# Kernel optimization log

Hardware: AMD Instinct MI355X
Metric: run time of the kernel (lower is better)

Reference implementation:

```python
import jax, jax.numpy as jnp
import numpy as np
import math

N_EMBD = 1024
N_HEAD = 16
HEAD_DIM = N_EMBD // N_HEAD // 2  # 32
DEPTH = 1
LAMBDA_INIT = 0.8 - 0.6 * math.exp(-0.3 * (DEPTH - 1))  # 0.2
EPS = 1e-5


def setup_inputs() -> dict:
    key = jax.random.key(0)
    ks = jax.random.split(key, 8)
    B, T, C = 4, 1024, N_EMBD
    x = jax.random.normal(ks[0], (B, T, C), dtype=jnp.float32)
    w_attn = jax.random.normal(ks[1], (C, 3 * C), dtype=jnp.float32) * (1.0 / math.sqrt(C))
    w_proj = jax.random.normal(ks[2], (C, C), dtype=jnp.float32) * (1.0 / math.sqrt(C))
    lambda_q1 = jax.random.normal(ks[3], (HEAD_DIM,), dtype=jnp.float32) * 0.1
    lambda_q2 = jax.random.normal(ks[4], (HEAD_DIM,), dtype=jnp.float32) * 0.1
    lambda_k1 = jax.random.normal(ks[5], (HEAD_DIM,), dtype=jnp.float32) * 0.1
    lambda_k2 = jax.random.normal(ks[6], (HEAD_DIM,), dtype=jnp.float32) * 0.1
    gamma = jnp.ones((2 * HEAD_DIM,), dtype=jnp.float32)  # RMSNorm affine weight
    return {"x": x, "w_attn": w_attn, "w_proj": w_proj,
            "lambda_q1": lambda_q1, "lambda_q2": lambda_q2,
            "lambda_k1": lambda_k1, "lambda_k2": lambda_k2, "gamma": gamma}


def reference(x, w_attn, w_proj, lambda_q1, lambda_q2, lambda_k1, lambda_k2, gamma):
    B, T, C = x.shape
    H, hd = N_HEAD, HEAD_DIM
    qkv = x @ w_attn                                  # [B,T,3C]
    q, k, v = jnp.split(qkv, 3, axis=-1)
    q = q.reshape(B, T, 2 * H, hd).transpose(0, 2, 1, 3)   # [B,2H,T,hd]
    k = k.reshape(B, T, 2 * H, hd).transpose(0, 2, 1, 3)   # [B,2H,T,hd]
    v = v.reshape(B, T, H, 2 * hd).transpose(0, 2, 1, 3)   # [B,H,T,2hd]
    q = q * (hd ** -0.5)
    att = jnp.einsum('bhtd,bhsd->bhts', q, k) * (1.0 / math.sqrt(hd))
    causal = jnp.tril(jnp.ones((T, T), dtype=bool))
    att = jnp.where(causal, att, -jnp.inf)
    att = jax.nn.softmax(att, axis=-1)                # [B,2H,T,T]
    lam1 = jnp.exp(jnp.sum(lambda_q1 * lambda_k1))
    lam2 = jnp.exp(jnp.sum(lambda_q2 * lambda_k2))
    lambda_full = lam1 - lam2 + LAMBDA_INIT
    att = att.reshape(B, H, 2, T, T)
    att = att[:, :, 0] - lambda_full * att[:, :, 1]   # [B,H,T,T]
    out = jnp.einsum('bhts,bhsd->bhtd', att, v)       # [B,H,T,2hd]
    # RMSNorm over last dim with affine weight
    rms = jax.lax.rsqrt(jnp.mean(out * out, axis=-1, keepdims=True) + EPS)
    out = out * rms * gamma
    out = (1.0 - LAMBDA_INIT) * out
    out = out.transpose(0, 2, 1, 3).reshape(B, T, C)
    return out @ w_proj
```

## Files before the change

kernel.cpp:

```cpp
#include <hip/hip_runtime.h>

typedef unsigned short u16;
typedef unsigned int u32;
typedef __bf16 bf16x8 __attribute__((ext_vector_type(8)));
typedef float f32x4 __attribute__((ext_vector_type(4)));
typedef u16 u16x8 __attribute__((ext_vector_type(8)));
typedef u16 u16x4 __attribute__((ext_vector_type(4)));

#define DEV static __device__ __forceinline__

struct MaskT { static constexpr bool value = true; };
struct NoMaskT { static constexpr bool value = false; };

DEV u16 f2bf(float f) {
  unsigned u = __builtin_bit_cast(unsigned, f);
  u += 0x7fffu + ((u >> 16) & 1u);
  return (u16)(u >> 16);
}
DEV u16 f2bf_fast(float f) {
  unsigned u = __builtin_bit_cast(unsigned, f);
  return (u16)((u + 0x8000u) >> 16);
}
DEV float fexp2(float x) {
  float r;
  asm("v_exp_f32 %0, %1" : "=v"(r) : "v"(x));
  return r;
}

DEV void gld16(const void* g, void* l) {
  __builtin_amdgcn_global_load_lds((__attribute__((address_space(1))) void*)(g),
                                   (__attribute__((address_space(3))) void*)(l),
                                   16, 0, 0);
}

__global__ __launch_bounds__(256) void k_cast(const float* __restrict__ in,
                                              u16* __restrict__ out, int n4) {
  int i = blockIdx.x * 256 + threadIdx.x;
  if (i >= n4) return;
  float4 v = ((const float4*)in)[i];
  u16x4 r = { f2bf(v.x), f2bf(v.y), f2bf(v.z), f2bf(v.w) };
  ((u16x4*)out)[i] = r;
}

__global__ __launch_bounds__(256) void k_transpose_cast(const float* __restrict__ in,
                                                        u16* __restrict__ out,
                                                        int R, int Cc) {
  __shared__ u16 tile[64][65];
  int r0 = blockIdx.x * 64, c0 = blockIdx.y * 64;
  int tid = threadIdx.x;
#pragma unroll
  for (int rr = 0; rr < 4; ++rr) {
    int r = rr * 16 + (tid >> 4);
    int c = (tid & 15) * 4;
    float4 v = *(const float4*)&in[(size_t)(r0 + r) * Cc + c0 + c];
    tile[r][c + 0] = f2bf(v.x); tile[r][c + 1] = f2bf(v.y);
    tile[r][c + 2] = f2bf(v.z); tile[r][c + 3] = f2bf(v.w);
  }
  __syncthreads();
#pragma unroll
  for (int rr = 0; rr < 2; ++rr) {
    int cr = rr * 32 + (tid >> 3);
    int rc = (tid & 7) * 8;
    u16x8 v;
#pragma unroll
    for (int j = 0; j < 8; ++j) v[j] = tile[rc + j][cr];
    *(u16x8*)&out[(size_t)(c0 + cr) * R + r0 + rc] = v;
  }
}

__global__ __launch_bounds__(256) void k_vtrans(const u16* __restrict__ qkv,
                                                u16* __restrict__ vt) {
  __shared__ u16 tile[64][65];
  int bid = blockIdx.x;
  int b = bid >> 8, h = (bid >> 4) & 15, tt = bid & 15;
  int tid = threadIdx.x;
#pragma unroll
  for (int rr = 0; rr < 2; ++rr) {
    int tl = rr * 32 + (tid >> 3);
    int d0 = (tid & 7) * 8;
    u16x8 v = *(const u16x8*)&qkv[(size_t)(b * 1024 + tt * 64 + tl) * 3072 + 2048 + h * 64 + d0];
#pragma unroll
    for (int j = 0; j < 8; ++j) tile[tl][d0 + j] = v[j];
  }
  __syncthreads();
#pragma unroll
  for (int rr = 0; rr < 2; ++rr) {
    int d = rr * 32 + (tid >> 3);
    int t0 = (tid & 7) * 8;
    u16x8 v;
#pragma unroll
    for (int j = 0; j < 8; ++j) v[j] = tile[t0 + j][d];
    *(u16x8*)&vt[((size_t)(b * 16 + h) * 64 + d) * 1024 + tt * 64 + t0] = v;
  }
}

__global__ void k_lambda(const float* lq1, const float* lq2,
                         const float* lk1, const float* lk2, float* out) {
  int i = threadIdx.x;
  float a = 0.f, b = 0.f;
  if (i < 32) { a = lq1[i] * lk1[i]; b = lq2[i] * lk2[i]; }
#pragma unroll
  for (int s = 1; s < 64; s <<= 1) { a += __shfl_xor(a, s); b += __shfl_xor(b, s); }
  if (i == 0) out[0] = __expf(a) - __expf(b) + 0.2f;
}

template <bool OUT_F32>
__global__ __launch_bounds__(256) void k_gemm(const u16* __restrict__ A,
                                              const u16* __restrict__ Bt,
                                              void* __restrict__ Cout,
                                              int M, int N, int K) {
  __shared__ __align__(16) u16 As[2][128 * 32];
  __shared__ __align__(16) u16 Bs[2][128 * 32];
  int tid = threadIdx.x;
  int nbn = N >> 7;
  int wg = ((int)blockIdx.x & 7) * ((int)gridDim.x >> 3) + ((int)blockIdx.x >> 3);
  int bm = wg / nbn, bn = wg % nbn;
  int m0 = bm << 7, n0 = bn << 7;
  int lane = tid & 63, w = tid >> 6, wm = w >> 1, wn = w & 1;
  int lr = lane & 15, lg = lane >> 4;
  const u16* pA0; const u16* pA1; const u16* pB0; const u16* pB1;
  {
    int i0 = tid, i1 = tid + 256;
    int r0 = i0 >> 2, s80 = (i0 & 3) ^ ((r0 >> 1) & 3);
    int r1 = i1 >> 2, s81 = (i1 & 3) ^ ((r1 >> 1) & 3);
    pA0 = &A[(size_t)(m0 + r0) * K + s80 * 8];
    pA1 = &A[(size_t)(m0 + r1) * K + s81 * 8];
    pB0 = &Bt[(size_t)(n0 + r0) * K + s80 * 8];
    pB1 = &Bt[(size_t)(n0 + r1) * K + s81 * 8];
  }
  f32x4 acc[4][4] = {};
  auto stage = [&](int kt, int buf) {
    gld16(pA0 + kt, &As[buf][tid * 8]);
    gld16(pA1 + kt, &As[buf][(tid + 256) * 8]);
    gld16(pB0 + kt, &Bs[buf][tid * 8]);
    gld16(pB1 + kt, &Bs[buf][(tid + 256) * 8]);
  };
  int NK = K >> 5;
  stage(0, 0);
  for (int ki = 0; ki < NK; ++ki) {
    int cur = ki & 1;
    if (ki + 1 < NK) {
      stage((ki + 1) << 5, cur ^ 1);
      asm volatile("s_waitcnt vmcnt(4)" ::: "memory");
    } else {
      asm volatile("s_waitcnt vmcnt(0)" ::: "memory");
    }
    __builtin_amdgcn_s_barrier();
    __builtin_amdgcn_sched_barrier(0);
    bf16x8 af[4], bfr[4];
#pragma unroll
    for (int m = 0; m < 4; ++m) {
      int r = wm * 64 + m * 16 + lr;
      int c8 = lg ^ ((r >> 1) & 3);
      af[m] = *(const bf16x8*)&As[cur][r * 32 + c8 * 8];
    }
#pragma unroll
    for (int n = 0; n < 4; ++n) {
      int r = wn * 64 + n * 16 + lr;
      int c8 = lg ^ ((r >> 1) & 3);
      bfr[n] = *(const bf16x8*)&Bs[cur][r * 32 + c8 * 8];
    }
#pragma unroll
    for (int m = 0; m < 4; ++m)
#pragma unroll
      for (int n = 0; n < 4; ++n)
        acc[m][n] = __builtin_amdgcn_mfma_f32_16x16x32_bf16(af[m], bfr[n], acc[m][n], 0, 0, 0);
    __builtin_amdgcn_sched_barrier(0);
    __builtin_amdgcn_s_barrier();
  }
#pragma unroll
  for (int m = 0; m < 4; ++m)
#pragma unroll
    for (int r = 0; r < 4; ++r) {
      int gr = m0 + wm * 64 + m * 16 + lg * 4 + r;
#pragma unroll
      for (int n = 0; n < 4; ++n) {
        int gc = n0 + wn * 64 + n * 16 + lr;
        if (OUT_F32) ((float*)Cout)[(size_t)gr * N + gc] = acc[m][n][r];
        else ((u16*)Cout)[(size_t)gr * N + gc] = f2bf(acc[m][n][r]);
      }
    }
}

__global__ __launch_bounds__(256) void k_diffattn(const u16* __restrict__ qkv,
                                                  const u16* __restrict__ vt,
                                                  const float* __restrict__ lam_p,
                                                  const float* __restrict__ gamma,
                                                  u16* __restrict__ attn_out) {
  __shared__ __align__(16) u16 Ks[2][2][64 * 32];
  __shared__ __align__(16) u16 Vs[2][64 * 64];
  __shared__ __align__(16) u16 Ps[4][2][16 * 72];
  int bid = blockIdx.x;
  int p = bid >> 6, b = (bid >> 4) & 3, h = bid & 15;
  int tid = threadIdx.x, lane = tid & 63, w = tid >> 6;
  int lr = lane & 15, lg = lane >> 4;
  int g1 = 2 * h, g2 = g1 + 1;
  float lam = *lam_p;
  const float cexp = 0.045084222f;
  f32x4 zero = {0.f, 0.f, 0.f, 0.f};
  u16* P1 = &Ps[w][0][0];
  u16* P2 = &Ps[w][1][0];

  const u16* pK1; const u16* pK2;
  {
    int r = tid >> 2, c8 = tid & 3;
    int s8 = c8 ^ ((r >> 1) & 3);
    size_t krow = (size_t)(b * 1024 + r) * 3072 + 1024;
    pK1 = qkv + krow + g1 * 32 + s8 * 8;
    pK2 = qkv + krow + g2 * 32 + s8 * 8;
  }
  const u16* pV0; const u16* pV1;
  {
    const u16* vbase = vt + ((size_t)(b * 16 + h) * 64) * 1024;
    int d0 = tid >> 3, o0 = (tid & 7) ^ (d0 & 7);
    int d1 = d0 + 32;
    pV0 = vbase + (size_t)d0 * 1024 + o0 * 8;
    pV1 = vbase + (size_t)d1 * 1024 + o0 * 8;
  }

  auto stage = [&](int s0, int buf) {
    gld16(pK1 + (size_t)s0 * 3072, &Ks[buf][0][tid * 8]);
    gld16(pK2 + (size_t)s0 * 3072, &Ks[buf][1][tid * 8]);
    gld16(pV0 + s0, &Vs[buf][tid * 8]);
    gld16(pV1 + s0, &Vs[buf][(tid + 256) * 8]);
  };

  auto phase = [&](int qb) {
    int q0 = qb * 64;
    size_t qrow = (size_t)(b * 1024 + q0 + w * 16 + lr);
    bf16x8 qf1 = *(const bf16x8*)&qkv[qrow * 3072 + g1 * 32 + lg * 8];
    bf16x8 qf2 = *(const bf16x8*)&qkv[qrow * 3072 + g2 * 32 + lg * 8];
    f32x4 o1[4] = {}, o2[4] = {};
    float l1[4] = {}, l2[4] = {};
    int qg_base = q0 + w * 16 + lg * 4;

    auto tile = [&](int cur, int s0, auto mk) {
      f32x4 s1[4], s2[4];
#pragma unroll
      for (int ni = 0; ni < 4; ++ni) {
        int rk = ni * 16 + lr;
        int c8 = lg ^ ((rk >> 1) & 3);
        bf16x8 kf1 = *(const bf16x8*)&Ks[cur][0][rk * 32 + c8 * 8];
        bf16x8 kf2 = *(const bf16x8*)&Ks[cur][1][rk * 32 + c8 * 8];
        s1[ni] = __builtin_amdgcn_mfma_f32_16x16x32_bf16(qf1, kf1, zero, 0, 0, 0);
        s2[ni] = __builtin_amdgcn_mfma_f32_16x16x32_bf16(qf2, kf2, zero, 0, 0, 0);
      }
#pragma unroll
      for (int ni = 0; ni < 4; ++ni) {
        int sg = s0 + ni * 16 + lr;
#pragma unroll
        for (int r = 0; r < 4; ++r) {
          float v1 = fexp2(s1[ni][r] * cexp);
          float v2 = fexp2(s2[ni][r] * cexp);
          if constexpr (decltype(mk)::value) {
            if (sg > qg_base + r) { v1 = 0.f; v2 = 0.f; }
          }
          l1[r] += v1; l2[r] += v2;
          P1[(lg * 4 + r) * 72 + ni * 16 + lr] = f2bf_fast(v1);
          P2[(lg * 4 + r) * 72 + ni * 16 + lr] = f2bf_fast(v2);
        }
      }
#pragma unroll
      for (int kk = 0; kk < 2; ++kk) {
        bf16x8 pa1 = *(const bf16x8*)&P1[lr * 72 + kk * 32 + lg * 8];
        bf16x8 pa2 = *(const bf16x8*)&P2[lr * 72 + kk * 32 + lg * 8];
#pragma unroll
        for (int ni = 0; ni < 4; ++ni) {
          int d = ni * 16 + lr;
          int c8 = (kk * 4 + lg) ^ (d & 7);
          bf16x8 vb = *(const bf16x8*)&Vs[cur][d * 64 + c8 * 8];
          o1[ni] = __builtin_amdgcn_mfma_f32_16x16x32_bf16(pa1, vb, o1[ni], 0, 0, 0);
          o2[ni] = __builtin_amdgcn_mfma_f32_16x16x32_bf16(pa2, vb, o2[ni], 0, 0, 0);
        }
      }
    };

    stage(0, 0);
    for (int t = 0; t < qb; ++t) {
      int cur = t & 1;
      stage((t + 1) * 64, cur ^ 1);
      asm volatile("s_waitcnt vmcnt(4)" ::: "memory");
      __builtin_amdgcn_s_barrier();
      __builtin_amdgcn_sched_barrier(0);
      tile(cur, t * 64, NoMaskT{});
      __builtin_amdgcn_sched_barrier(0);
      __builtin_amdgcn_s_barrier();
    }
    asm volatile("s_waitcnt vmcnt(0)" ::: "memory");
    __builtin_amdgcn_s_barrier();
    __builtin_amdgcn_sched_barrier(0);
    tile(qb & 1, q0, MaskT{});

#pragma unroll
    for (int r = 0; r < 4; ++r) {
      l1[r] += __shfl_xor(l1[r], 1); l1[r] += __shfl_xor(l1[r], 2);
      l1[r] += __shfl_xor(l1[r], 4); l1[r] += __shfl_xor(l1[r], 8);
      l2[r] += __shfl_xor(l2[r], 1); l2[r] += __shfl_xor(l2[r], 2);
      l2[r] += __shfl_xor(l2[r], 4); l2[r] += __shfl_xor(l2[r], 8);
    }
    float inv1[4], inv2[4];
#pragma unroll
    for (int r = 0; r < 4; ++r) { inv1[r] = 1.f / l1[r]; inv2[r] = 1.f / l2[r]; }
    float val[4][4];
#pragma unroll
    for (int ni = 0; ni < 4; ++ni)
#pragma unroll
      for (int r = 0; r < 4; ++r)
        val[ni][r] = o1[ni][r] * inv1[r] - lam * (o2[ni][r] * inv2[r]);
#pragma unroll
    for (int r = 0; r < 4; ++r) {
      float ss = 0.f;
#pragma unroll
      for (int ni = 0; ni < 4; ++ni) ss += val[ni][r] * val[ni][r];
      ss += __shfl_xor(ss, 1); ss += __shfl_xor(ss, 2);
      ss += __shfl_xor(ss, 4); ss += __shfl_xor(ss, 8);
      float sc = rsqrtf(ss * (1.f / 64.f) + 1e-5f) * 0.8f;
#pragma unroll
      for (int ni = 0; ni < 4; ++ni) val[ni][r] *= sc;
    }
#pragma unroll
    for (int ni = 0; ni < 4; ++ni) {
      int d = ni * 16 + lr;
      float g = gamma[d];
#pragma unroll
      for (int r = 0; r < 4; ++r) {
        int trow = q0 + w * 16 + lg * 4 + r;
        attn_out[(size_t)(b * 1024 + trow) * 1024 + h * 64 + d] = f2bf(val[ni][r] * g);
      }
    }
  };

  phase(p);
  __syncthreads();
  phase(15 - p);
}

extern "C" void kernel_launch(void* const* d_in, const int* in_sizes, int n_in,
                              void* d_out, int out_size, void* d_ws, size_t ws_size,
                              hipStream_t stream) {
  const float* x   = (const float*)d_in[0];
  const float* wa  = (const float*)d_in[1];
  const float* wp  = (const float*)d_in[2];
  const float* lq1 = (const float*)d_in[3];
  const float* lq2 = (const float*)d_in[4];
  const float* lk1 = (const float*)d_in[5];
  const float* lk2 = (const float*)d_in[6];
  const float* gam = (const float*)d_in[7];
  float* out = (float*)d_out;

  char* ws = (char*)d_ws;
  u16* xb   = (u16*)(ws);
  u16* wab  = (u16*)(ws + (8ull << 20));
  u16* wpb  = (u16*)(ws + (14ull << 20));
  u16* qkv  = (u16*)(ws + (16ull << 20));
  u16* vt   = (u16*)(ws + (40ull << 20));
  u16* aout = (u16*)(ws + (48ull << 20));
  float* lam = (float*)(ws + (56ull << 20));

  k_cast<<<4096, 256, 0, stream>>>(x, xb, 1024 * 1024);
  k_transpose_cast<<<dim3(16, 48), 256, 0, stream>>>(wa, wab, 1024, 3072);
  k_transpose_cast<<<dim3(16, 16), 256, 0, stream>>>(wp, wpb, 1024, 1024);
  k_lambda<<<1, 64, 0, stream>>>(lq1, lq2, lk1, lk2, lam);
  k_gemm<false><<<32 * 24, 256, 0, stream>>>(xb, wab, qkv, 4096, 3072, 1024);
  k_vtrans<<<1024, 256, 0, stream>>>(qkv, vt);
  k_diffattn<<<512, 256, 0, stream>>>(qkv, vt, lam, gam, aout);
  k_gemm<true><<<32 * 8, 256, 0, stream>>>(aout, wpb, out, 4096, 1024, 1024);
}
```

Before: 191.4 us.

## Process both causal query blocks in a single shared K/V sweep

The attention kernel used to handle its two query blocks (p and 15-p) one after the other, reloading K/V tiles for each. Now one loop over K/V tiles feeds both blocks: the short block stops after its masked diagonal tile and the long block continues alone. This removes duplicate K/V staging and barrier rounds, and interleaves independent MFMA work from both blocks for more instruction-level parallelism. The cost is doubled accumulator registers and a second P buffer in LDS, which may lower occupancy. The block-index-to-p mapping is also reordered.

```diff
diff --git a/kernel.cpp b/kernel.cpp
--- a/kernel.cpp
+++ b/kernel.cpp
@@ -9,8 +9,8 @@
 
 #define DEV static __device__ __forceinline__
 
-struct MaskT { static constexpr bool value = true; };
-struct NoMaskT { static constexpr bool value = false; };
+template <bool B> struct BC { static constexpr bool value = B; };
+template <int I> struct IC { static constexpr int value = I; };
 
 DEV u16 f2bf(float f) {
   unsigned u = __builtin_bit_cast(unsigned, f);
@@ -189,17 +189,18 @@
                                                   u16* __restrict__ attn_out) {
   __shared__ __align__(16) u16 Ks[2][2][64 * 32];
   __shared__ __align__(16) u16 Vs[2][64 * 64];
-  __shared__ __align__(16) u16 Ps[4][2][16 * 72];
+  __shared__ __align__(16) u16 Ps[2][4][2][16 * 72];
   int bid = blockIdx.x;
-  int p = bid >> 6, b = (bid >> 4) & 3, h = bid & 15;
+  int kk8 = (bid & 255) >> 6;
+  int p = (bid >> 8) ? (7 - kk8) : kk8;
+  int b = (bid >> 4) & 3, h = bid & 15;
+  int qbS = p, qbL = 15 - p;
   int tid = threadIdx.x, lane = tid & 63, w = tid >> 6;
   int lr = lane & 15, lg = lane >> 4;
   int g1 = 2 * h, g2 = g1 + 1;
   float lam = *lam_p;
   const float cexp = 0.045084222f;
   f32x4 zero = {0.f, 0.f, 0.f, 0.f};
-  u16* P1 = &Ps[w][0][0];
-  u16* P2 = &Ps[w][1][0];
 
   const u16* pK1; const u16* pK2;
   {
@@ -213,11 +214,9 @@
   {
     const u16* vbase = vt + ((size_t)(b * 16 + h) * 64) * 1024;
     int d0 = tid >> 3, o0 = (tid & 7) ^ (d0 & 7);
-    int d1 = d0 + 32;
     pV0 = vbase + (size_t)d0 * 1024 + o0 * 8;
-    pV1 = vbase + (size_t)d1 * 1024 + o0 * 8;
-  }
-
+    pV1 = vbase + (size_t)(d0 + 32) * 1024 + o0 * 8;
+  }
   auto stage = [&](int s0, int buf) {
     gld16(pK1 + (size_t)s0 * 3072, &Ks[buf][0][tid * 8]);
     gld16(pK2 + (size_t)s0 * 3072, &Ks[buf][1][tid * 8]);
@@ -225,88 +224,111 @@
     gld16(pV1 + s0, &Vs[buf][(tid + 256) * 8]);
   };
 
-  auto phase = [&](int qb) {
-    int q0 = qb * 64;
-    size_t qrow = (size_t)(b * 1024 + q0 + w * 16 + lr);
-    bf16x8 qf1 = *(const bf16x8*)&qkv[qrow * 3072 + g1 * 32 + lg * 8];
-    bf16x8 qf2 = *(const bf16x8*)&qkv[qrow * 3072 + g2 * 32 + lg * 8];
-    f32x4 o1[4] = {}, o2[4] = {};
-    float l1[4] = {}, l2[4] = {};
-    int qg_base = q0 + w * 16 + lg * 4;
-
-    auto tile = [&](int cur, int s0, auto mk) {
-      f32x4 s1[4], s2[4];
+  bf16x8 qf1[2], qf2[2];
+  f32x4 o1[2][4] = {}, o2[2][4] = {};
+  float l1[2][4] = {}, l2[2][4] = {};
+  int q0v[2] = {qbS * 64, qbL * 64};
+  int qg[2] = {q0v[0] + w * 16 + lg * 4, q0v[1] + w * 16 + lg * 4};
+  {
+    size_t qrowS = (size_t)(b * 1024 + q0v[0] + w * 16 + lr) * 3072;
+    size_t qrowL = (size_t)(b * 1024 + q0v[1] + w * 16 + lr) * 3072;
+    qf1[0] = *(const bf16x8*)&qkv[qrowS + g1 * 32 + lg * 8];
+    qf2[0] = *(const bf16x8*)&qkv[qrowS + g2 * 32 + lg * 8];
+    qf1[1] = *(const bf16x8*)&qkv[qrowL + g1 * 32 + lg * 8];
+    qf2[1] = *(const bf16x8*)&qkv[qrowL + g2 * 32 + lg * 8];
+  }
+  u16* P1[2] = {&Ps[0][w][0][0], &Ps[1][w][0][0]};
+  u16* P2[2] = {&Ps[0][w][1][0], &Ps[1][w][1][0]};
+
+  auto qk_sm = [&](auto qc, auto mk, int cur, int s0) {
+    constexpr int qi = decltype(qc)::value;
+    f32x4 s1[4], s2[4];
+#pragma unroll
+    for (int ni = 0; ni < 4; ++ni) {
+      int rk = ni * 16 + lr;
+      int c8 = lg ^ ((rk >> 1) & 3);
+      bf16x8 kf1 = *(const bf16x8*)&Ks[cur][0][rk * 32 + c8 * 8];
+      bf16x8 kf2 = *(const bf16x8*)&Ks[cur][1][rk * 32 + c8 * 8];
+      s1[ni] = __builtin_amdgcn_mfma_f32_16x16x32_bf16(qf1[qi], kf1, zero, 0, 0, 0);
+      s2[ni] = __builtin_amdgcn_mfma_f32_16x16x32_bf16(qf2[qi], kf2, zero, 0, 0, 0);
+    }
+#pragma unroll
+    for (int ni = 0; ni < 4; ++ni) {
+      int sg = s0 + ni * 16 + lr;
+#pragma unroll
+      for (int r = 0; r < 4; ++r) {
+        float v1 = fexp2(s1[ni][r] * cexp);
+        float v2 = fexp2(s2[ni][r] * cexp);
+        if constexpr (decltype(mk)::value) {
+          if (sg > qg[qi] + r) { v1 = 0.f; v2 = 0.f; }
+        }
+        l1[qi][r] += v1; l2[qi][r] += v2;
+        P1[qi][(lg * 4 + r) * 72 + ni * 16 + lr] = f2bf_fast(v1);
+        P2[qi][(lg * 4 + r) * 72 + ni * 16 + lr] = f2bf_fast(v2);
+      }
+    }
+  };
+  auto pv = [&](auto qc, int cur) {
+    constexpr int qi = decltype(qc)::value;
+#pragma unroll
+    for (int kk = 0; kk < 2; ++kk) {
+      bf16x8 pa1 = *(const bf16x8*)&P1[qi][lr * 72 + kk * 32 + lg * 8];
+      bf16x8 pa2 = *(const bf16x8*)&P2[qi][lr * 72 + kk * 32 + lg * 8];
 #pragma unroll
       for (int ni = 0; ni < 4; ++ni) {
-        int rk = ni * 16 + lr;
-        int c8 = lg ^ ((rk >> 1) & 3);
-        bf16x8 kf1 = *(const bf16x8*)&Ks[cur][0][rk * 32 + c8 * 8];
-        bf16x8 kf2 = *(const bf16x8*)&Ks[cur][1][rk * 32 + c8 * 8];
-        s1[ni] = __builtin_amdgcn_mfma_f32_16x16x32_bf16(qf1, kf1, zero, 0, 0, 0);
-        s2[ni] = __builtin_amdgcn_mfma_f32_16x16x32_bf16(qf2, kf2, zero, 0, 0, 0);
+        int d = ni * 16 + lr;
+        int c8 = (kk * 4 + lg) ^ (d & 7);
+        bf16x8 vb = *(const bf16x8*)&Vs[cur][d * 64 + c8 * 8];
+        o1[qi][ni] = __builtin_amdgcn_mfma_f32_16x16x32_bf16(pa1, vb, o1[qi][ni], 0, 0, 0);
+        o2[qi][ni] = __builtin_amdgcn_mfma_f32_16x16x32_bf16(pa2, vb, o2[qi][ni], 0, 0, 0);
       }
-#pragma unroll
-      for (int ni = 0; ni < 4; ++ni) {
-        int sg = s0 + ni * 16 + lr;
-#pragma unroll
-        for (int r = 0; r < 4; ++r) {
-          float v1 = fexp2(s1[ni][r] * cexp);
-          float v2 = fexp2(s2[ni][r] * cexp);
-          if constexpr (decltype(mk)::value) {
-            if (sg > qg_base + r) { v1 = 0.f; v2 = 0.f; }
-          }
-          l1[r] += v1; l2[r] += v2;
-          P1[(lg * 4 + r) * 72 + ni * 16 + lr] = f2bf_fast(v1);
-          P2[(lg * 4 + r) * 72 + ni * 16 + lr] = f2bf_fast(v2);
-        }
-      }
-#pragma unroll
-      for (int kk = 0; kk < 2; ++kk) {
-        bf16x8 pa1 = *(const bf16x8*)&P1[lr * 72 + kk * 32 + lg * 8];
-        bf16x8 pa2 = *(const bf16x8*)&P2[lr * 72 + kk * 32 + lg * 8];
-#pragma unroll
-        for (int ni = 0; ni < 4; ++ni) {
-          int d = ni * 16 + lr;
-          int c8 = (kk * 4 + lg) ^ (d & 7);
-          bf16x8 vb = *(const bf16x8*)&Vs[cur][d * 64 + c8 * 8];
-          o1[ni] = __builtin_amdgcn_mfma_f32_16x16x32_bf16(pa1, vb, o1[ni], 0, 0, 0);
-          o2[ni] = __builtin_amdgcn_mfma_f32_16x16x32_bf16(pa2, vb, o2[ni], 0, 0, 0);
-        }
-      }
-    };
-
-    stage(0, 0);
-    for (int t = 0; t < qb; ++t) {
-      int cur = t & 1;
+    }
+  };
+
+  auto step = [&](int t, auto doS, auto mkS, auto mkL) {
+    int cur = t & 1;
+    if (t < qbL) {
       stage((t + 1) * 64, cur ^ 1);
       asm volatile("s_waitcnt vmcnt(4)" ::: "memory");
-      __builtin_amdgcn_s_barrier();
-      __builtin_amdgcn_sched_barrier(0);
-      tile(cur, t * 64, NoMaskT{});
-      __builtin_amdgcn_sched_barrier(0);
-      __builtin_amdgcn_s_barrier();
-    }
-    asm volatile("s_waitcnt vmcnt(0)" ::: "memory");
+    } else {
+      asm volatile("s_waitcnt vmcnt(0)" ::: "memory");
+    }
     __builtin_amdgcn_s_barrier();
     __builtin_amdgcn_sched_barrier(0);
-    tile(qb & 1, q0, MaskT{});
-
+    int s0 = t * 64;
+    if constexpr (decltype(doS)::value) qk_sm(IC<0>{}, mkS, cur, s0);
+    qk_sm(IC<1>{}, mkL, cur, s0);
+    if constexpr (decltype(doS)::value) pv(IC<0>{}, cur);
+    pv(IC<1>{}, cur);
+    __builtin_amdgcn_sched_barrier(0);
+    __builtin_amdgcn_s_barrier();
+  };
+
+  stage(0, 0);
+  int t = 0;
+  for (; t < qbS; ++t) step(t, BC<true>{}, BC<false>{}, BC<false>{});
+  step(t, BC<true>{}, BC<true>{}, BC<false>{});
+  ++t;
+  for (; t < qbL; ++t) step(t, BC<false>{}, BC<false>{}, BC<false>{});
+  step(t, BC<false>{}, BC<false>{}, BC<true>{});
+
+  auto epi = [&](auto qc) {
+    constexpr int qi = decltype(qc)::value;
 #pragma unroll
     for (int r = 0; r < 4; ++r) {
-      l1[r] += __shfl_xor(l1[r], 1); l1[r] += __shfl_xor(l1[r], 2);
-      l1[r] += __shfl_xor(l1[r], 4); l1[r] += __shfl_xor(l1[r], 8);
-      l2[r] += __shfl_xor(l2[r], 1); l2[r] += __shfl_xor(l2[r], 2);
-      l2[r] += __shfl_xor(l2[r], 4); l2[r] += __shfl_xor(l2[r], 8);
-    }
-    float inv1[4], inv2[4];
-#pragma unroll
-    for (int r = 0; r < 4; ++r) { inv1[r] = 1.f / l1[r]; inv2[r] = 1.f / l2[r]; }
+      float a = l1[qi][r], c = l2[qi][r];
+      a += __shfl_xor(a, 1); a += __shfl_xor(a, 2);
+      a += __shfl_xor(a, 4); a += __shfl_xor(a, 8);
+      c += __shfl_xor(c, 1); c += __shfl_xor(c, 2);
+      c += __shfl_xor(c, 4); c += __shfl_xor(c, 8);
+      l1[qi][r] = a; l2[qi][r] = c;
+    }
     float val[4][4];
 #pragma unroll
     for (int ni = 0; ni < 4; ++ni)
 #pragma unroll
       for (int r = 0; r < 4; ++r)
-        val[ni][r] = o1[ni][r] * inv1[r] - lam * (o2[ni][r] * inv2[r]);
+        val[ni][r] = o1[qi][ni][r] * (1.f / l1[qi][r]) - lam * (o2[qi][ni][r] * (1.f / l2[qi][r]));
 #pragma unroll
     for (int r = 0; r < 4; ++r) {
       float ss = 0.f;
@@ -324,15 +346,13 @@
       float g = gamma[d];
 #pragma unroll
       for (int r = 0; r < 4; ++r) {
-        int trow = q0 + w * 16 + lg * 4 + r;
+        int trow = q0v[qi] + w * 16 + lg * 4 + r;
         attn_out[(size_t)(b * 1024 + trow) * 1024 + h * 64 + d] = f2bf(val[ni][r] * g);
       }
     }
   };
-
-  phase(p);
-  __syncthreads();
-  phase(15 - p);
+  epi(IC<0>{});
+  epi(IC<1>{});
 }
 
 extern "C" void kernel_launch(void* const* d_in, const int* in_sizes, int n_in,
```

Measured after the change: 204.7 us. 6.9% more time.
